# Performance work log

Measured on AMD Instinct MI355X. Metric: run time of the kernel, lower is better.

The kernel has to match this reference:

```python
import jax, jax.numpy as jnp
import numpy as np

L, B = 512, 512
IN, OBS, K, S = 16, 16, 64, 64


def _lin(x, w, b):
    return x @ w.T + b


def _preprocess(x, w1, b1, w2, b2):
    # PreProcess: two fc layers with ReLU (TD-VAE style)
    return jax.nn.relu(_lin(jax.nn.relu(_lin(x, w1, b1)), w2, b2))


def _dblock(x, p):
    # DBlock: t = tanh(fc1(x)) * sigmoid(fc2(x)); returns (mu, logsigma)
    fc1_w, fc1_b, fc2_w, fc2_b, mu_w, mu_b, ls_w, ls_b = p
    t = jnp.tanh(_lin(x, fc1_w, fc1_b)) * jax.nn.sigmoid(_lin(x, fc2_w, fc2_b))
    return _lin(t, mu_w, mu_b), _lin(t, ls_w, ls_b)


def setup_inputs() -> dict:
    key = jax.random.key(0)
    keys = iter(jax.random.split(key, 64))

    def W(shape, fan_in):
        s = 1.0 / np.sqrt(fan_in)
        return jax.random.uniform(next(keys), shape, jnp.float32, -s, s)

    inp = {
        'external_input_seq': jax.random.normal(next(keys), (L, B, IN), jnp.float32),
        'observations_seq': jax.random.normal(next(keys), (L, B, OBS), jnp.float32),
        'noise': jax.random.normal(next(keys), (L, B, S), jnp.float32),
        # process_u / process_x (PreProcess)
        'pu_w1': W((K, IN), IN), 'pu_b1': W((K,), IN), 'pu_w2': W((K, K), K), 'pu_b2': W((K,), K),
        'px_w1': W((K, OBS), OBS), 'px_b1': W((K,), OBS), 'px_w2': W((K, K), K), 'px_b2': W((K,), K),
        # input_rnn: vanilla tanh RNN(k, k), 1 layer
        'rnn_wih': W((K, K), K), 'rnn_whh': W((K, K), K), 'rnn_bih': W((K,), K), 'rnn_bhh': W((K,), K),
        # posterior_a_layer: MLP(2k, k, k, 1)
        'a_w1': W((K, 2 * K), 2 * K), 'a_b1': W((K,), 2 * K), 'a_w2': W((K, K), K), 'a_b2': W((K,), K),
        # posterior_gauss: DBlock(state+k, 2k, state)
        'po_fc1_w': W((2 * K, S + K), S + K), 'po_fc1_b': W((2 * K,), S + K),
        'po_fc2_w': W((2 * K, S + K), S + K), 'po_fc2_b': W((2 * K,), S + K),
        'po_mu_w': W((S, 2 * K), 2 * K), 'po_mu_b': W((S,), 2 * K),
        'po_ls_w': W((S, 2 * K), 2 * K), 'po_ls_b': W((S,), 2 * K),
        # prior_gauss: DBlock(state+k, 2k, state)
        'pr_fc1_w': W((2 * K, S + K), S + K), 'pr_fc1_b': W((2 * K,), S + K),
        'pr_fc2_w': W((2 * K, S + K), S + K), 'pr_fc2_b': W((2 * K,), S + K),
        'pr_mu_w': W((S, 2 * K), 2 * K), 'pr_mu_b': W((S,), 2 * K),
        'pr_ls_w': W((S, 2 * K), 2 * K), 'pr_ls_b': W((S,), 2 * K),
    }
    return inp


def reference(external_input_seq, observations_seq, noise,
              pu_w1, pu_b1, pu_w2, pu_b2, px_w1, px_b1, px_w2, px_b2,
              rnn_wih, rnn_whh, rnn_bih, rnn_bhh,
              a_w1, a_b1, a_w2, a_b2,
              po_fc1_w, po_fc1_b, po_fc2_w, po_fc2_b, po_mu_w, po_mu_b, po_ls_w, po_ls_b,
              pr_fc1_w, pr_fc1_b, pr_fc2_w, pr_fc2_b, pr_mu_w, pr_mu_b, pr_ls_w, pr_ls_b):
    l, b, _ = external_input_seq.shape
    k = rnn_whh.shape[0]
    s = po_mu_w.shape[0]

    u_emb = _preprocess(external_input_seq, pu_w1, pu_b1, pu_w2, pu_b2)   # [l,b,k]
    x_emb = _preprocess(observations_seq, px_w1, px_b1, px_w2, px_b2)     # [l,b,k]

    # input_rnn: tanh RNN over time (seq-first), h0 = 0
    def rnn_step(h, x):
        h = jnp.tanh(x @ rnn_wih.T + rnn_bih + h @ rnn_whh.T + rnn_bhh)
        return h, h
    _, d_seq = jax.lax.scan(rnn_step, jnp.zeros((b, k), u_emb.dtype), u_emb)  # [l,b,k]

    # posterior_a_layer: pointwise MLP; flip+flip around a pointwise map is identity
    a_in = jnp.concatenate([d_seq, x_emb], axis=-1)                       # [l,b,2k]
    a_seq = _lin(jnp.tanh(_lin(a_in, a_w1, a_b1)), a_w2, a_b2)            # [l,b,k]

    po = (po_fc1_w, po_fc1_b, po_fc2_w, po_fc2_b, po_mu_w, po_mu_b, po_ls_w, po_ls_b)
    pr = (pr_fc1_w, pr_fc1_b, pr_fc2_w, pr_fc2_b, pr_mu_w, pr_mu_b, pr_ls_w, pr_ls_b)

    # sequential latent update + reparameterized sampling
    def step(z_prev, inputs):
        a_t, d_t, eps_t = inputs
        res_mu, logsigma = _dblock(jnp.concatenate([z_prev, a_t], axis=-1), po)
        mu = _dblock(jnp.concatenate([z_prev, d_t], axis=-1), pr)[0] + res_mu
        # cov = diag(exp(logsigma)) => std = exp(0.5 * logsigma)
        z = mu + jnp.exp(0.5 * logsigma) * eps_t
        return z, (mu, logsigma, z)

    z0 = jnp.zeros((b, s), u_emb.dtype)
    _, (state_mu, state_logsigma, sampled_state) = jax.lax.scan(step, z0, (a_seq, d_seq, noise))
    return state_mu, state_logsigma, sampled_state, d_seq
```

## Files before the change

kernel.cpp:

```cpp
#include <hip/hip_runtime.h>

typedef unsigned short u16;
typedef unsigned int u32;

#define L 512
#define BB 512
#define NROWS (L*BB)
#define CH (NROWS*64)

enum {
  O_PUW1 = 0,
  O_PUB1 = 1024,
  O_PUW2 = 1088,
  O_PUB2 = 5184,
  O_PXW1 = 5248,
  O_PXB1 = 6272,
  O_PXW2 = 6336,
  O_PXB2 = 10432,
  O_WIH  = 10496,
  O_RNB  = 14592,
  O_WHH  = 14656,
  O_AW1  = 18752,
  O_AB1  = 26944,
  O_AW2  = 27008,
  O_AB2  = 31104,
  O_POF1 = 31168,
  O_POF1B= 47552,
  O_POF2 = 47680,
  O_POF2B= 64064,
  O_POMU = 64192,
  O_POMUB= 72384,
  O_POLS = 72448,
  O_POLSB= 80640,
  O_PRF1 = 80704,
  O_PRF1B= 97088,
  O_PRF2 = 97216,
  O_PRF2B= 113600,
  O_PRMU = 113728,
  O_PRMUB= 121920,
  O_FLAG = 121984,
  O_HB   = 122000
};
enum {
  HU1 = 0,
  HU2 = 1024,
  HX1 = 5120,
  HX2 = 6144,
  HW3U= 10240,
  HW3X= 14336,
  HEND= 18432
};

__device__ __forceinline__ float b2f(u16 x){ return __uint_as_float(((u32)x)<<16); }
__device__ __forceinline__ u16 f2b(float f){
  u32 u = __float_as_uint(f);
  u32 r = (u + 0x7fffu + ((u>>16)&1u)) >> 16;
  return (u16)r;
}

#if __has_builtin(__builtin_amdgcn_exp2f)
#define EXP2(x) __builtin_amdgcn_exp2f(x)
#else
#define EXP2(x) exp2f(x)
#endif
#if __has_builtin(__builtin_amdgcn_rcpf)
#define RCP(x) __builtin_amdgcn_rcpf(x)
#else
#define RCP(x) (1.0f/(x))
#endif

__device__ __forceinline__ float tanhf_fast(float x){
  float e = EXP2(x * 2.8853900817779268f);
  return 1.0f - 2.0f * RCP(e + 1.0f);
}
__device__ __forceinline__ float sigm_fast(float x){
  float e = EXP2(-1.4426950408889634f * x);
  return RCP(1.0f + e);
}

__device__ __forceinline__ void bar_lds(){
  __builtin_amdgcn_sched_barrier(0);
  asm volatile("s_waitcnt lgkmcnt(0)" ::: "memory");
  __builtin_amdgcn_s_barrier();
  __builtin_amdgcn_sched_barrier(0);
}

typedef __attribute__((ext_vector_type(8))) __bf16 bf16x8;
typedef __attribute__((ext_vector_type(4))) float f32x4;

__device__ __forceinline__ f32x4 mfma16(bf16x8 a, bf16x8 b, f32x4 c){
  return __builtin_amdgcn_mfma_f32_16x16x32_bf16(a, b, c, 0, 0, 0);
}
__device__ __forceinline__ bf16x8 wfrag(const float* W, int off){
  union { short s[8]; bf16x8 v; } c;
#pragma unroll
  for (int i=0;i<8;i++) c.s[i] = (short)f2b(W[off+i]);
  return c.v;
}
__device__ __forceinline__ bf16x8 load16(const u16* p){
  union { uint4 u; bf16x8 v; } c;
  c.u = *(const uint4*)p;
  return c.v;
}
__device__ __forceinline__ bf16x8 zfrag(){
  union { uint4 u; bf16x8 v; } c;
  c.u = make_uint4(0,0,0,0);
  return c.v;
}
__device__ __forceinline__ bf16x8 ldA64(const u32* buf, int r, int s){
  union { uint4 u; bf16x8 v; } c;
  c.u = ((const uint4*)buf)[r*8 + (s ^ (r&7))];
  return c.v;
}
__device__ __forceinline__ bf16x8 ldT(const u32* buf, int r, int s){
  union { uint4 u; bf16x8 v; } c;
  c.u = ((const uint4*)buf)[r*16 + (s ^ (r&7))];
  return c.v;
}

template<int MODE>
__device__ __forceinline__ float ldOne(const void* p, size_t i){
  if constexpr (MODE) return ((const float*)p)[i];
  else return b2f(((const u16*)p)[i]);
}
template<int MODE>
__device__ __forceinline__ void stOne(void* p, size_t i, float v){
  if constexpr (MODE) ((float*)p)[i] = v;
  else ((u16*)p)[i] = f2b(v);
}
template<int MODE>
__device__ __forceinline__ float wld(const void* p, int i){
  if constexpr (MODE) return ((const float*)p)[i];
  else return b2f(((const u16*)p)[i]);
}
template<int MODE>
__device__ __forceinline__ u16 hld(const void* p, int i){
  if constexpr (MODE) return f2b(((const float*)p)[i]);
  else return ((const u16*)p)[i];
}
template<int MODE>
__device__ __forceinline__ void* chunkp(void* out, int j){
  return (void*)((char*)out + (size_t)j * (size_t)CH * (MODE ? 4 : 2));
}
__device__ __forceinline__ bool live(const float* W, int tag){
  return ((const u32*)W)[O_FLAG] == (u32)tag;
}

__global__ void kprobe(const u32* __restrict__ ext, u32* __restrict__ flagp){
  if (threadIdx.x == 0 && blockIdx.x == 0){
    int cnt = 0;
    for (int i = 0; i < 1024; ++i){
      u32 e = (ext[i] >> 7) & 0xFFu;
      cnt += (e >= 110u && e <= 134u) ? 1 : 0;
    }
    flagp[0] = (cnt > 512) ? 1u : 2u;
  }
}

template<int MODE>
__global__ void k0_convert(
  const void* pu_w1, const void* pu_b1, const void* pu_w2, const void* pu_b2,
  const void* px_w1, const void* px_b1, const void* px_w2, const void* px_b2,
  const void* rnn_wih, const void* rnn_whh, const void* rnn_bih, const void* rnn_bhh,
  const void* a_w1, const void* a_b1, const void* a_w2, const void* a_b2,
  const void* po_f1, const void* po_f1b, const void* po_f2, const void* po_f2b,
  const void* po_mu, const void* po_mub, const void* po_ls, const void* po_lsb,
  const void* pr_f1, const void* pr_f1b, const void* pr_f2, const void* pr_f2b,
  const void* pr_mu, const void* pr_mub,
  float* W)
{
  if (!live(W, MODE ? 2 : 1)) return;
  const int g = blockIdx.x*blockDim.x + threadIdx.x;
  const int gs = gridDim.x*blockDim.x;
#define CVT(off, src, n) for (int i=g;i<(n);i+=gs) W[(off)+i] = wld<MODE>(src,i);
  CVT(O_PUW1, pu_w1, 1024)  CVT(O_PUB1, pu_b1, 64)
  CVT(O_PUW2, pu_w2, 4096)  CVT(O_PUB2, pu_b2, 64)
  CVT(O_PXW1, px_w1, 1024)  CVT(O_PXB1, px_b1, 64)
  CVT(O_PXW2, px_w2, 4096)  CVT(O_PXB2, px_b2, 64)
  CVT(O_WIH,  rnn_wih, 4096)
  CVT(O_WHH,  rnn_whh, 4096)
  CVT(O_AW1,  a_w1, 8192)   CVT(O_AB1, a_b1, 64)
  CVT(O_AW2,  a_w2, 4096)   CVT(O_AB2, a_b2, 64)
  CVT(O_POF1, po_f1, 16384) CVT(O_POF1B, po_f1b, 128)
  CVT(O_POF2, po_f2, 16384) CVT(O_POF2B, po_f2b, 128)
  CVT(O_POMU, po_mu, 8192)  CVT(O_POMUB, po_mub, 64)
  CVT(O_POLS, po_ls, 8192)  CVT(O_POLSB, po_lsb, 64)
  CVT(O_PRF1, pr_f1, 16384) CVT(O_PRF1B, pr_f1b, 128)
  CVT(O_PRF2, pr_f2, 16384) CVT(O_PRF2B, pr_f2b, 128)
  CVT(O_PRMU, pr_mu, 8192)  CVT(O_PRMUB, pr_mub, 64)
#undef CVT
  for (int i=g;i<64;i+=gs) W[O_RNB+i] = wld<MODE>(rnn_bih,i) + wld<MODE>(rnn_bhh,i);

  u16* Wh = (u16*)(W + O_HB);
  for (int i=g;i<1024;i+=gs) Wh[HU1+i] = hld<MODE>(pu_w1,i);
  for (int i=g;i<4096;i+=gs) Wh[HU2+i] = hld<MODE>(pu_w2,i);
  for (int i=g;i<1024;i+=gs) Wh[HX1+i] = hld<MODE>(px_w1,i);
  for (int i=g;i<4096;i+=gs) Wh[HX2+i] = hld<MODE>(px_w2,i);
  for (int i=g;i<4096;i+=gs) Wh[HW3U+i] = hld<MODE>(rnn_wih,i);
  for (int i=g;i<4096;i+=gs){
    int j = i>>6, c = i&63;
    Wh[HW3X+i] = hld<MODE>(a_w1, j*128 + 64 + c);
  }
}

#define K1_NT 4
template<int MODE>
__global__ __launch_bounds__(512) void k1m(
  const void* __restrict__ ext, const void* __restrict__ obs,
  const float* __restrict__ W, void* __restrict__ outb)
{
  if (!live(W, MODE ? 2 : 1)) return;
  void* rnn_in = chunkp<MODE>(outb, 1);
  void* ax_out = chunkp<MODE>(outb, 2);

  const int tid = threadIdx.x;
  const int wave = tid>>6, lane = tid&63;
  const int lr = lane&15, lg = lane>>4;
  const u16* Wh = (const u16*)(W + O_HB);

  __shared__ __align__(16) u16 Et[8][1024];
  u16* myT = Et[wave];
  u32* myT32 = (u32*)myT;

#pragma unroll 1
  for (int p=0;p<2;p++){
    const void* src = p ? obs : ext;
    void* dst = p ? ax_out : rnn_in;
    const int h1 = p?HX1:HU1, h2 = p?HX2:HU2, h3 = p?HW3X:HW3U;
    const int b1o = p?O_PXB1:O_PUB1, b2o = p?O_PXB2:O_PUB2, b3o = p?O_AB1:O_RNB;

    bf16x8 w1[4], w2[4][2], w3[4][2];
    float bb1[4], bb2[4], bb3[4];
#pragma unroll
    for (int n=0;n<4;n++){
      const int j = n*16 + lr;
      w1[n] = (lg<2) ? load16(Wh + h1 + j*16 + lg*8) : zfrag();
#pragma unroll
      for (int kk=0;kk<2;kk++){
        w2[n][kk] = load16(Wh + h2 + j*64 + kk*32 + lg*8);
        w3[n][kk] = load16(Wh + h3 + j*64 + kk*32 + lg*8);
      }
      bb1[n] = W[b1o+j]; bb2[n] = W[b2o+j]; bb3[n] = W[b3o+j];
    }

#pragma unroll 1
    for (int it=0; it<K1_NT; ++it){
      const size_t row0 = ((size_t)(blockIdx.x*8 + wave)*K1_NT + it)*16;

      bf16x8 xa;
      if (lg < 2){
        if constexpr (MODE){
          const float4* sp = (const float4*)((const float*)src + (row0+lr)*16);
          float4 f0 = sp[lg*2], f1 = sp[lg*2+1];
          union { short s[8]; bf16x8 v; } c;
          c.s[0]=(short)f2b(f0.x); c.s[1]=(short)f2b(f0.y);
          c.s[2]=(short)f2b(f0.z); c.s[3]=(short)f2b(f0.w);
          c.s[4]=(short)f2b(f1.x); c.s[5]=(short)f2b(f1.y);
          c.s[6]=(short)f2b(f1.z); c.s[7]=(short)f2b(f1.w);
          xa = c.v;
        } else {
          xa = load16((const u16*)src + (row0+lr)*16 + lg*8);
        }
      } else xa = zfrag();

      f32x4 c[4];
#pragma unroll
      for (int n=0;n<4;n++){
        f32x4 ci = {bb1[n],bb1[n],bb1[n],bb1[n]};
        ci = mfma16(xa, w1[n], ci);
#pragma unroll
        for (int r=0;r<4;r++){
          float v = fmaxf(ci[r], 0.0f);
          const int b = lg*4 + r, j = n*16 + lr;
          myT[b*64 + (((j>>3)^(b&7))<<3) + (j&7)] = f2b(v);
        }
      }
      {
        bf16x8 a0 = ldA64(myT32, lr, lg);
        bf16x8 a1 = ldA64(myT32, lr, 4+lg);
#pragma unroll
        for (int n=0;n<4;n++){
          f32x4 ci = {bb2[n],bb2[n],bb2[n],bb2[n]};
          ci = mfma16(a0, w2[n][0], ci);
          ci = mfma16(a1, w2[n][1], ci);
          c[n] = ci;
        }
#pragma unroll
        for (int n=0;n<4;n++)
#pragma unroll
          for (int r=0;r<4;r++){
            float v = fmaxf(c[n][r], 0.0f);
            const int b = lg*4 + r, j = n*16 + lr;
            myT[b*64 + (((j>>3)^(b&7))<<3) + (j&7)] = f2b(v);
          }
      }
      {
        bf16x8 a0 = ldA64(myT32, lr, lg);
        bf16x8 a1 = ldA64(myT32, lr, 4+lg);
#pragma unroll
        for (int n=0;n<4;n++){
          f32x4 ci = {bb3[n],bb3[n],bb3[n],bb3[n]};
          ci = mfma16(a0, w3[n][0], ci);
          ci = mfma16(a1, w3[n][1], ci);
          c[n] = ci;
        }
#pragma unroll
        for (int n=0;n<4;n++)
#pragma unroll
          for (int r=0;r<4;r++){
            const int b = lg*4 + r, j = n*16 + lr;
            myT[b*64 + (((j>>3)^(b&7))<<3) + (j&7)] = f2b(c[n][r]);
          }
      }
#pragma unroll
      for (int s2=0;s2<2;s2++){
        const int s_lin = lane*2 + s2;
        const int r = s_lin>>3, sl = s_lin&7;
        uint4 v = ((const uint4*)myT32)[r*8 + (sl^(r&7))];
        if constexpr (MODE){
          float* dp = (float*)dst + (row0+r)*64 + sl*8;
          u32 w[4] = {v.x, v.y, v.z, v.w};
          float f[8];
#pragma unroll
          for (int i=0;i<4;i++){ f[2*i] = b2f((u16)(w[i]&0xffffu)); f[2*i+1] = b2f((u16)(w[i]>>16)); }
          ((float4*)dp)[0] = make_float4(f[0],f[1],f[2],f[3]);
          ((float4*)dp)[1] = make_float4(f[4],f[5],f[6],f[7]);
        } else {
          ((uint4*)((u16*)dst + (row0+r)*64))[sl] = v;
        }
      }
    }
  }
}

__device__ __forceinline__ float dot16(const float* w, float4 a, float4 b, float4 c, float4 d){
  float s0=0.f, s1=0.f;
  s0=fmaf(w[0],a.x,s0);  s1=fmaf(w[1],a.y,s1);  s0=fmaf(w[2],a.z,s0);  s1=fmaf(w[3],a.w,s1);
  s0=fmaf(w[4],b.x,s0);  s1=fmaf(w[5],b.y,s1);  s0=fmaf(w[6],b.z,s0);  s1=fmaf(w[7],b.w,s1);
  s0=fmaf(w[8],c.x,s0);  s1=fmaf(w[9],c.y,s1);  s0=fmaf(w[10],c.z,s0); s1=fmaf(w[11],c.w,s1);
  s0=fmaf(w[12],d.x,s0); s1=fmaf(w[13],d.y,s1); s0=fmaf(w[14],d.z,s0); s1=fmaf(w[15],d.w,s1);
  return s0+s1;
}

template<int MODE>
__global__ __launch_bounds__(256) void k2_rnn(
  const float* __restrict__ W, void* __restrict__ outb)
{
  if (!live(W, MODE ? 2 : 1)) return;
  void* a_seq  = chunkp<MODE>(outb, 0);
  void* rnn_in = chunkp<MODE>(outb, 1);
  void* ax     = chunkp<MODE>(outb, 2);
  void* d_seq  = chunkp<MODE>(outb, 3);

  const int b = blockIdx.x;
  const int tid = threadIdx.x;
  const int q = tid>>6, j = tid&63;

  float wh[16], wa1[16], wa2[16];
#pragma unroll
  for (int i=0;i<16;i++){
    wh[i]  = W[O_WHH + j*64  + q*16 + i];
    wa1[i] = W[O_AW1 + j*128 + q*16 + i];
    wa2[i] = W[O_AW2 + j*64  + q*16 + i];
  }
  const float ab2j = W[O_AB2 + j];

  __shared__ __align__(16) float h_lds[64];
  __shared__ __align__(16) float v_lds[64];
  __shared__ __align__(16) float red1[256], red2[256], red3[256];
  if (tid < 64){ h_lds[tid] = 0.f; v_lds[tid] = 0.f; }

  const size_t brow = (size_t)b*64 + j;
  float pre = 0.f;
  if (q==0) pre = ldOne<MODE>(rnn_in, brow);
  __syncthreads();

  for (int t=0; t<L+2; ++t){
    const float4* hv = (const float4*)(&h_lds[q*16]);
    const float4* vv = (const float4*)(&v_lds[q*16]);
    float4 h0=hv[0], h1=hv[1], h2=hv[2], h3=hv[3];
    float4 v0=vv[0], v1=vv[1], v2=vv[2], v3=vv[3];
    red1[tid] = dot16(wh,  h0,h1,h2,h3);
    red2[tid] = dot16(wa1, h0,h1,h2,h3);
    red3[tid] = dot16(wa2, v0,v1,v2,v3);
    bar_lds();
    if (q==0){
      if (t < L){
        const size_t idx = (size_t)t*(BB*64) + brow;
        float s = red1[j]+red1[64+j]+red1[128+j]+red1[192+j] + pre;
        float hn = tanhf_fast(s);
        h_lds[j] = hn;
        stOne<MODE>(d_seq, idx, hn);
      }
      if (t+1 < L) pre = ldOne<MODE>(rnn_in, (size_t)(t+1)*(BB*64) + brow);
    } else if (q==1){
      if (t>=1 && t<=L){
        const size_t idx = (size_t)(t-1)*(BB*64) + brow;
        float s = red2[j]+red2[64+j]+red2[128+j]+red2[192+j] + pre;
        v_lds[j] = tanhf_fast(s);
      }
      if (t < L) pre = ldOne<MODE>(ax, (size_t)t*(BB*64) + brow);
    } else if (q==2){
      if (t>=2){
        const size_t idx = (size_t)(t-2)*(BB*64) + brow;
        float s = red3[j]+red3[64+j]+red3[128+j]+red3[192+j] + ab2j;
        stOne<MODE>(a_seq, idx, s);
      }
    }
    bar_lds();
  }
}

template<int MODE>
__global__ __launch_bounds__(512,2) void k4m(
  const float* __restrict__ W,
  const void* __restrict__ noise, void* __restrict__ outb)
{
  if (!live(W, MODE ? 2 : 1)) return;
  void* amu = chunkp<MODE>(outb, 0);
  void* lsc = chunkp<MODE>(outb, 1);
  void* zc  = chunkp<MODE>(outb, 2);
  void* dsq = chunkp<MODE>(outb, 3);

  const int G = blockIdx.x;
  const int tid = threadIdx.x;
  const int wave = tid>>6, lane = tid&63;
  const int lr = lane&15, lg = lane>>4;

  __shared__ __align__(16) u32 Zbuf[512];
  __shared__ __align__(16) u32 Abuf[2][512];
  __shared__ __align__(16) u32 Dbuf[2][512];
  __shared__ __align__(16) u32 Ebuf[2][1024];
  __shared__ __align__(16) u32 Tpo[1024];
  __shared__ __align__(16) u32 Tpr[1024];
  __shared__ __align__(16) float Obuf[3*1024];
  __shared__ float bmu[64], bls[64];

  const bool isPo = wave < 4;
  const int wq = wave & 3;
  const int jA = wq*32;

  const int of1 = isPo ? O_POF1 : O_PRF1;
  const int of2 = isPo ? O_POF2 : O_PRF2;
  bf16x8 wf1[2][4], wf2[2][4];
  float bA1[2], bA2[2];
#pragma unroll
  for (int nt=0; nt<2; ++nt){
    const int j = jA + nt*16 + lr;
    bA1[nt] = W[(isPo?O_POF1B:O_PRF1B) + j];
    bA2[nt] = W[(isPo?O_POF2B:O_PRF2B) + j];
#pragma unroll
    for (int kk=0; kk<4; ++kk){
      const int k = kk*32 + lg*8;
      wf1[nt][kk] = wfrag(W, of1 + j*128 + k);
      wf2[nt][kk] = wfrag(W, of2 + j*128 + k);
    }
  }
  const int mb = wave>>1, nh = wave&1;
  bf16x8 wb[2][4];
  if (wave < 6){
    const int ob = (mb==0) ? O_POMU : (mb==1 ? O_POLS : O_PRMU);
#pragma unroll
    for (int nt=0; nt<2; ++nt)
#pragma unroll
      for (int kk=0; kk<4; ++kk){
        const int j = nh*32 + nt*16 + lr;
        const int k = kk*32 + lg*8;
        wb[nt][kk] = wfrag(W, ob + j*128 + k);
      }
  }

  if (tid < 64){ bmu[tid] = W[O_POMUB+tid] + W[O_PRMUB+tid]; bls[tid] = W[O_POLSB+tid]; }
  Zbuf[tid & 511] = 0;

  const int pr_ = lane>>2, pc = lane&3;
  float4 pA[4], pE[4]; uint4 qA[2], qE[2];

  auto pf_issue = [&](int tt){
    const size_t rowb = ((size_t)tt*BB + G*16 + pr_)*64;
    const void* gsrc = (wave==6) ? amu : dsq;
    if constexpr (MODE){
      const float4* sp = (const float4*)((const float*)gsrc + rowb) + pc*4;
#pragma unroll
      for (int i=0;i<4;i++) pA[i] = sp[i];
      if (wave==6){
        const float4* ep = (const float4*)((const float*)noise + rowb) + pc*4;
#pragma unroll
        for (int i=0;i<4;i++) pE[i] = ep[i];
      }
    } else {
      const uint4* sp = (const uint4*)((const u16*)gsrc + rowb) + pc*2;
      qA[0] = sp[0]; qA[1] = sp[1];
      if (wave==6){
        const uint4* ep = (const uint4*)((const u16*)noise + rowb) + pc*2;
        qE[0] = ep[0]; qE[1] = ep[1];
      }
    }
  };
  auto pf_write = [&](int buf){
    u32* dst = (wave==6) ? Abuf[buf] : Dbuf[buf];
    uint4* d0 = (uint4*)dst + (pr_*8 + ((pc*2  ) ^ (pr_&7)));
    uint4* d1 = (uint4*)dst + (pr_*8 + ((pc*2+1) ^ (pr_&7)));
    if constexpr (MODE){
      u32 w[8];
#pragma unroll
      for (int i=0;i<4;i++){
        w[2*i]   = (u32)f2b(pA[i].x) | ((u32)f2b(pA[i].y)<<16);
        w[2*i+1] = (u32)f2b(pA[i].z) | ((u32)f2b(pA[i].w)<<16);
      }
      *d0 = make_uint4(w[0],w[1],w[2],w[3]);
      *d1 = make_uint4(w[4],w[5],w[6],w[7]);
      if (wave==6){
        uint4* eb = (uint4*)Ebuf[buf] + (pr_*16 + pc*4);
#pragma unroll
        for (int i=0;i<4;i++){
          union { float4 f; uint4 u; } cv; cv.f = pE[i];
          eb[i] = cv.u;
        }
      }
    } else {
      *d0 = qA[0]; *d1 = qA[1];
      if (wave==6){
        u32* Eb = Ebuf[buf] + pr_*64 + pc*16;
        u32 ww[4] = {qE[0].x, qE[0].y, qE[0].z, qE[0].w};
#pragma unroll
        for (int i=0;i<4;i++){ Eb[2*i] = ww[i]<<16; Eb[2*i+1] = ww[i] & 0xffff0000u; }
        u32 w2[4] = {qE[1].x, qE[1].y, qE[1].z, qE[1].w};
#pragma unroll
        for (int i=0;i<4;i++){ Eb[8+2*i] = w2[i]<<16; Eb[8+2*i+1] = w2[i] & 0xffff0000u; }
      }
    }
  };

  if (wave >= 6){
    pf_issue(0); pf_write(0);
    if (L > 1) pf_issue(1);
  }
  __syncthreads();

  for (int t=0; t<L; ++t){
    const int cur = t&1, nb = cur^1;

    const u32* ADc = isPo ? Abuf[cur] : Dbuf[cur];
    bf16x8 a0 = ldA64(Zbuf, lr, lg);
    bf16x8 a1 = ldA64(Zbuf, lr, 4+lg);
    bf16x8 a2 = ldA64(ADc,  lr, lg);
    bf16x8 a3 = ldA64(ADc,  lr, 4+lg);
    f32x4 c1[2], c2[2];
#pragma unroll
    for (int nt=0; nt<2; ++nt){
      f32x4 i1 = {bA1[nt],bA1[nt],bA1[nt],bA1[nt]};
      f32x4 i2 = {bA2[nt],bA2[nt],bA2[nt],bA2[nt]};
      i1 = mfma16(a0, wf1[nt][0], i1);
      i1 = mfma16(a1, wf1[nt][1], i1);
      i1 = mfma16(a2, wf1[nt][2], i1);
      i1 = mfma16(a3, wf1[nt][3], i1);
      i2 = mfma16(a0, wf2[nt][0], i2);
      i2 = mfma16(a1, wf2[nt][1], i2);
      i2 = mfma16(a2, wf2[nt][2], i2);
      i2 = mfma16(a3, wf2[nt][3], i2);
      c1[nt] = i1; c2[nt] = i2;
    }
    u16* Td = (u16*)(isPo ? Tpo : Tpr);
#pragma unroll
    for (int nt=0; nt<2; ++nt)
#pragma unroll
      for (int r=0; r<4; ++r){
        float tv = tanhf_fast(c1[nt][r]) * sigm_fast(c2[nt][r]);
        const int j = jA + nt*16 + lr;
        const int b = lg*4 + r;
        Td[b*128 + (((j>>3)^(b&7))<<3) + (j&7)] = f2b(tv);
      }
    bar_lds();

    if (wave < 6){
      const u32* Ts = (mb==2) ? Tpr : Tpo;
      bf16x8 t0 = ldT(Ts, lr, lg);
      bf16x8 t1 = ldT(Ts, lr, 4+lg);
      bf16x8 t2 = ldT(Ts, lr, 8+lg);
      bf16x8 t3 = ldT(Ts, lr, 12+lg);
      f32x4 d0 = {0.f,0.f,0.f,0.f}, d1 = {0.f,0.f,0.f,0.f};
      d0 = mfma16(t0, wb[0][0], d0);
      d0 = mfma16(t1, wb[0][1], d0);
      d0 = mfma16(t2, wb[0][2], d0);
      d0 = mfma16(t3, wb[0][3], d0);
      d1 = mfma16(t0, wb[1][0], d1);
      d1 = mfma16(t1, wb[1][1], d1);
      d1 = mfma16(t2, wb[1][2], d1);
      d1 = mfma16(t3, wb[1][3], d1);
      float* Od = &Obuf[mb*1024];
#pragma unroll
      for (int r=0; r<4; ++r){
        const int b = lg*4 + r;
        const int j0 = nh*32 + lr;
        const int j1 = nh*32 + 16 + lr;
        Od[b*64 + (((j0>>2)^(b&7))<<2) + (j0&3)] = d0[r];
        Od[b*64 + (((j1>>2)^(b&7))<<2) + (j1&3)] = d1[r];
      }
    } else if (t+1 < L){
      pf_write(nb);
      if (t+2 < L) pf_issue(t+2);
    }
    bar_lds();

    {
      const int b = tid>>5;
      const int j = (tid&31)*2;
      const int sidx = b*64 + (((j>>2)^(b&7))<<2) + (j&3);
      float2 vpo = *(const float2*)&Obuf[0*1024 + sidx];
      float2 vls = *(const float2*)&Obuf[1*1024 + sidx];
      float2 vpr = *(const float2*)&Obuf[2*1024 + sidx];
      float2 bm = *(const float2*)&bmu[j];
      float2 bl = *(const float2*)&bls[j];
      float e0 = __uint_as_float(Ebuf[cur][b*64 + j]);
      float e1 = __uint_as_float(Ebuf[cur][b*64 + j + 1]);
      float mu0 = vpo.x + vpr.x + bm.x;
      float mu1 = vpo.y + vpr.y + bm.y;
      float ls0 = vls.x + bl.x;
      float ls1 = vls.y + bl.y;
      float z0 = fmaf(EXP2(ls0*0.7213475204444817f), e0, mu0);
      float z1 = fmaf(EXP2(ls1*0.7213475204444817f), e1, mu1);
      Zbuf[b*32 + (((j>>3)^(b&7))<<2) + ((j&7)>>1)] = (u32)f2b(z0) | ((u32)f2b(z1)<<16);
      const size_t idx = ((size_t)t*BB + G*16 + b)*64 + j;
      if constexpr (MODE){
        *(float2*)((float*)amu + idx) = make_float2(mu0, mu1);
        *(float2*)((float*)lsc + idx) = make_float2(ls0, ls1);
        *(float2*)((float*)zc  + idx) = make_float2(z0, z1);
      } else {
        *(u32*)((u16*)amu + idx) = (u32)f2b(mu0) | ((u32)f2b(mu1)<<16);
        *(u32*)((u16*)lsc + idx) = (u32)f2b(ls0) | ((u32)f2b(ls1)<<16);
        *(u32*)((u16*)zc  + idx) = (u32)f2b(z0)  | ((u32)f2b(z1)<<16);
      }
    }
    bar_lds();
  }
}

extern "C" void kernel_launch(void* const* d_in, const int* in_sizes, int n_in,
                              void* d_out, int out_size, void* d_ws, size_t ws_size,
                              hipStream_t stream)
{
  (void)in_sizes; (void)n_in; (void)out_size; (void)ws_size;

  const void* ext   = d_in[0];
  const void* obs   = d_in[1];
  const void* noise = d_in[2];
  float* W = (float*)d_ws;

  kprobe<<<1,64,0,stream>>>((const u32*)ext, (u32*)W + O_FLAG);

#define K0ARGS \
    d_in[3],  d_in[4],  d_in[5],  d_in[6],  d_in[7],  d_in[8],  d_in[9],  d_in[10], \
    d_in[11], d_in[12], d_in[13], d_in[14], d_in[15], d_in[16], d_in[17], d_in[18], \
    d_in[19], d_in[20], d_in[21], d_in[22], d_in[23], d_in[24], d_in[25], d_in[26], \
    d_in[27], d_in[28], d_in[29], d_in[30], d_in[31], d_in[32], W

  k0_convert<0><<<64,256,0,stream>>>(K0ARGS);
  k0_convert<1><<<64,256,0,stream>>>(K0ARGS);
#undef K0ARGS

  k1m<0><<<NROWS/(8*K1_NT*16), 512, 0, stream>>>(ext, obs, W, d_out);
  k1m<1><<<NROWS/(8*K1_NT*16), 512, 0, stream>>>(ext, obs, W, d_out);

  k2_rnn<0><<<BB, 256, 0, stream>>>(W, d_out);
  k2_rnn<1><<<BB, 256, 0, stream>>>(W, d_out);

  k4m<0><<<32, 512, 0, stream>>>(W, noise, d_out);
  k4m<1><<<32, 512, 0, stream>>>(W, noise, d_out);
}
```

Baseline: 1.021 ms.

## Restructure RNN kernel into per-wave full dot products with double-buffered state

The RNN/posterior-a kernel now gives each of three wavefronts one whole 64-wide matrix row per lane, held in registers, instead of splitting each dot product across four waves and reducing through shared memory. The hidden and intermediate state vectors are double-buffered, so one barrier per timestep is enough instead of two, and the reduction-buffer traffic goes away. This shortens the sequential critical path per step. In exchange each lane holds 64 weights in registers, and the block uses fewer threads with more serial FMAs per lane.

```diff
diff --git a/kernel.cpp b/kernel.cpp
--- a/kernel.cpp
+++ b/kernel.cpp
@@ -333,17 +333,8 @@
   }
 }
 
-__device__ __forceinline__ float dot16(const float* w, float4 a, float4 b, float4 c, float4 d){
-  float s0=0.f, s1=0.f;
-  s0=fmaf(w[0],a.x,s0);  s1=fmaf(w[1],a.y,s1);  s0=fmaf(w[2],a.z,s0);  s1=fmaf(w[3],a.w,s1);
-  s0=fmaf(w[4],b.x,s0);  s1=fmaf(w[5],b.y,s1);  s0=fmaf(w[6],b.z,s0);  s1=fmaf(w[7],b.w,s1);
-  s0=fmaf(w[8],c.x,s0);  s1=fmaf(w[9],c.y,s1);  s0=fmaf(w[10],c.z,s0); s1=fmaf(w[11],c.w,s1);
-  s0=fmaf(w[12],d.x,s0); s1=fmaf(w[13],d.y,s1); s0=fmaf(w[14],d.z,s0); s1=fmaf(w[15],d.w,s1);
-  return s0+s1;
-}
-
-template<int MODE>
-__global__ __launch_bounds__(256) void k2_rnn(
+template<int MODE>
+__global__ __launch_bounds__(192) void k2f(
   const float* __restrict__ W, void* __restrict__ outb)
 {
   if (!live(W, MODE ? 2 : 1)) return;
@@ -354,57 +345,67 @@
 
   const int b = blockIdx.x;
   const int tid = threadIdx.x;
-  const int q = tid>>6, j = tid&63;
-
-  float wh[16], wa1[16], wa2[16];
-#pragma unroll
-  for (int i=0;i<16;i++){
-    wh[i]  = W[O_WHH + j*64  + q*16 + i];
-    wa1[i] = W[O_AW1 + j*128 + q*16 + i];
-    wa2[i] = W[O_AW2 + j*64  + q*16 + i];
-  }
-  const float ab2j = W[O_AB2 + j];
-
-  __shared__ __align__(16) float h_lds[64];
-  __shared__ __align__(16) float v_lds[64];
-  __shared__ __align__(16) float red1[256], red2[256], red3[256];
-  if (tid < 64){ h_lds[tid] = 0.f; v_lds[tid] = 0.f; }
+  const int wv = tid>>6, j = tid&63;
+
+  float w[64];
+  const int wbase = (wv==0) ? (O_WHH + j*64)
+                  : (wv==1) ? (O_AW1 + j*128)
+                  :           (O_AW2 + j*64);
+#pragma unroll
+  for (int i=0;i<64;i++) w[i] = W[wbase + i];
+  const float ab2j = (wv==2) ? W[O_AB2 + j] : 0.f;
+
+  __shared__ __align__(16) float h_lds[2][64];
+  __shared__ __align__(16) float v_lds[2][64];
+  if (tid < 64){ h_lds[0][tid]=0.f; h_lds[1][tid]=0.f; v_lds[0][tid]=0.f; v_lds[1][tid]=0.f; }
 
   const size_t brow = (size_t)b*64 + j;
   float pre = 0.f;
-  if (q==0) pre = ldOne<MODE>(rnn_in, brow);
+  if (wv==0)      pre = ldOne<MODE>(rnn_in, brow);
+  else if (wv==1) pre = ldOne<MODE>(ax, brow);
   __syncthreads();
 
+#pragma unroll 1
   for (int t=0; t<L+2; ++t){
-    const float4* hv = (const float4*)(&h_lds[q*16]);
-    const float4* vv = (const float4*)(&v_lds[q*16]);
-    float4 h0=hv[0], h1=hv[1], h2=hv[2], h3=hv[3];
-    float4 v0=vv[0], v1=vv[1], v2=vv[2], v3=vv[3];
-    red1[tid] = dot16(wh,  h0,h1,h2,h3);
-    red2[tid] = dot16(wa1, h0,h1,h2,h3);
-    red3[tid] = dot16(wa2, v0,v1,v2,v3);
-    bar_lds();
-    if (q==0){
+    if (wv==0){
       if (t < L){
-        const size_t idx = (size_t)t*(BB*64) + brow;
-        float s = red1[j]+red1[64+j]+red1[128+j]+red1[192+j] + pre;
-        float hn = tanhf_fast(s);
-        h_lds[j] = hn;
-        stOne<MODE>(d_seq, idx, hn);
-      }
-      if (t+1 < L) pre = ldOne<MODE>(rnn_in, (size_t)(t+1)*(BB*64) + brow);
-    } else if (q==1){
+        const float4* hp = (const float4*)h_lds[(t+1)&1];
+        float s0=pre, s1=0.f;
+#pragma unroll
+        for (int k=0;k<16;k++){
+          float4 hh = hp[k];
+          s0 = fmaf(w[4*k],   hh.x, s0); s1 = fmaf(w[4*k+1], hh.y, s1);
+          s0 = fmaf(w[4*k+2], hh.z, s0); s1 = fmaf(w[4*k+3], hh.w, s1);
+        }
+        float hn = tanhf_fast(s0+s1);
+        h_lds[t&1][j] = hn;
+        stOne<MODE>(d_seq, (size_t)t*(BB*64) + brow, hn);
+        if (t+1 < L) pre = ldOne<MODE>(rnn_in, (size_t)(t+1)*(BB*64) + brow);
+      }
+    } else if (wv==1){
       if (t>=1 && t<=L){
-        const size_t idx = (size_t)(t-1)*(BB*64) + brow;
-        float s = red2[j]+red2[64+j]+red2[128+j]+red2[192+j] + pre;
-        v_lds[j] = tanhf_fast(s);
-      }
-      if (t < L) pre = ldOne<MODE>(ax, (size_t)t*(BB*64) + brow);
-    } else if (q==2){
+        const float4* hp = (const float4*)h_lds[(t+1)&1];
+        float s0=pre, s1=0.f;
+#pragma unroll
+        for (int k=0;k<16;k++){
+          float4 hh = hp[k];
+          s0 = fmaf(w[4*k],   hh.x, s0); s1 = fmaf(w[4*k+1], hh.y, s1);
+          s0 = fmaf(w[4*k+2], hh.z, s0); s1 = fmaf(w[4*k+3], hh.w, s1);
+        }
+        v_lds[(t+1)&1][j] = tanhf_fast(s0+s1);
+        if (t < L) pre = ldOne<MODE>(ax, (size_t)t*(BB*64) + brow);
+      }
+    } else {
       if (t>=2){
-        const size_t idx = (size_t)(t-2)*(BB*64) + brow;
-        float s = red3[j]+red3[64+j]+red3[128+j]+red3[192+j] + ab2j;
-        stOne<MODE>(a_seq, idx, s);
+        const float4* vp = (const float4*)v_lds[t&1];
+        float s0=ab2j, s1=0.f;
+#pragma unroll
+        for (int k=0;k<16;k++){
+          float4 vvv = vp[k];
+          s0 = fmaf(w[4*k],   vvv.x, s0); s1 = fmaf(w[4*k+1], vvv.y, s1);
+          s0 = fmaf(w[4*k+2], vvv.z, s0); s1 = fmaf(w[4*k+3], vvv.w, s1);
+        }
+        stOne<MODE>(a_seq, (size_t)(t-2)*(BB*64) + brow, s0+s1);
       }
     }
     bar_lds();
@@ -662,8 +663,8 @@
   k1m<0><<<NROWS/(8*K1_NT*16), 512, 0, stream>>>(ext, obs, W, d_out);
   k1m<1><<<NROWS/(8*K1_NT*16), 512, 0, stream>>>(ext, obs, W, d_out);
 
-  k2_rnn<0><<<BB, 256, 0, stream>>>(W, d_out);
-  k2_rnn<1><<<BB, 256, 0, stream>>>(W, d_out);
+  k2f<0><<<BB, 192, 0, stream>>>(W, d_out);
+  k2f<1><<<BB, 192, 0, stream>>>(W, d_out);
 
   k4m<0><<<32, 512, 0, stream>>>(W, noise, d_out);
   k4m<1><<<32, 512, 0, stream>>>(W, noise, d_out);
```

Measured after the change: 1.149 ms. +12.5%, slower.
